# Performance work log

Measured on AMD Instinct MI355X. Metric: run time of the kernel, lower is better.

The kernel has to match this reference:

```python
import jax, jax.numpy as jnp
import numpy as np

B, IN_SEQ, TGT_SEQ = 128, 50, 25
IN_SIZE, OUT_SIZE, RNN = 128, 128, 2048


def setup_inputs() -> dict:
    key = jax.random.key(0)
    ks = jax.random.split(key, 10)
    s_in = 1.0 / np.sqrt(IN_SIZE)
    s_out = 1.0 / np.sqrt(OUT_SIZE)
    s_rnn = 1.0 / np.sqrt(RNN)
    return {
        "encoder_inputs": jax.random.normal(ks[0], (B, IN_SEQ, IN_SIZE), jnp.float32),
        "decoder_inputs": jax.random.normal(ks[1], (B, TGT_SEQ, IN_SIZE), jnp.float32),
        "fc1_w": jax.random.uniform(ks[2], (OUT_SIZE, IN_SIZE), jnp.float32, -s_in, s_in),
        "fc1_b": jax.random.uniform(ks[3], (OUT_SIZE,), jnp.float32, -s_in, s_in),
        "w_ih": jax.random.uniform(ks[4], (3 * RNN, OUT_SIZE), jnp.float32, -s_rnn, s_rnn),
        "w_hh": jax.random.uniform(ks[5], (3 * RNN, RNN), jnp.float32, -s_rnn, s_rnn),
        "b_ih": jax.random.uniform(ks[6], (3 * RNN,), jnp.float32, -s_rnn, s_rnn),
        "b_hh": jax.random.uniform(ks[7], (3 * RNN,), jnp.float32, -s_rnn, s_rnn),
        "fc2_w": jax.random.uniform(ks[8], (OUT_SIZE, RNN), jnp.float32, -s_rnn, s_rnn),
        "fc2_b": jax.random.uniform(ks[9], (OUT_SIZE,), jnp.float32, -s_rnn, s_rnn),
    }


def _gru_cell(x, h, w_ih, w_hh, b_ih, b_hh):
    # PyTorch GRUCell: gates ordered (r, z, n)
    gi = x @ w_ih.T + b_ih            # [B, 3R]
    gh = h @ w_hh.T + b_hh            # [B, 3R]
    i_r, i_z, i_n = jnp.split(gi, 3, axis=-1)
    h_r, h_z, h_n = jnp.split(gh, 3, axis=-1)
    r = jax.nn.sigmoid(i_r + h_r)
    z = jax.nn.sigmoid(i_z + h_z)
    n = jnp.tanh(i_n + r * h_n)
    return (1.0 - z) * n + z * h


def reference(encoder_inputs, decoder_inputs, fc1_w, fc1_b, w_ih, w_hh, b_ih, b_hh, fc2_w, fc2_b):
    # Eval mode: F.dropout(training=False) is identity.
    enc = encoder_inputs @ fc1_w.T + fc1_b              # [B, S_in, OUT]
    enc_t = jnp.transpose(enc, (1, 0, 2))               # time-major [S_in, B, OUT]
    h0 = jnp.zeros((encoder_inputs.shape[0], RNN), enc.dtype)

    def enc_step(state, x):
        return _gru_cell(x, state, w_ih, w_hh, b_ih, b_hh), None

    state, _ = jax.lax.scan(enc_step, h0, enc_t[:-1])   # input_seq - 1 steps

    def dec_step(carry, _):
        state, inp = carry
        inp = jax.lax.stop_gradient(inp)                # inp.detach()
        state = _gru_cell(inp, state, w_ih, w_hh, b_ih, b_hh)
        out = inp + state @ fc2_w.T + fc2_b             # residual decoder
        return (state, out), out

    _, outs = jax.lax.scan(dec_step, (state, enc_t[-1]), None, length=TGT_SEQ)
    return jnp.transpose(outs, (1, 0, 2))               # [B, TGT_SEQ, OUT]
```

## Files before the change

kernel.cpp:

```cpp
#include <hip/hip_runtime.h>
#include <limits.h>

constexpr int kB   = 128;
constexpr int kSin = 50;
constexpr int kT   = 25;
constexpr int kD   = 128;
constexpr int kR   = 2048;
constexpr int kNB  = 256;
constexpr int kNT  = 512;
constexpr int kRing = 8;

typedef __bf16 bf16x8 __attribute__((ext_vector_type(8)));
typedef float  f32x4  __attribute__((ext_vector_type(4)));
typedef unsigned short u16;
typedef unsigned long long u64;

__device__ __forceinline__ float bf2f(u16 u){ union{unsigned i; float f;}x; x.i=((unsigned)u)<<16; return x.f; }
__device__ __forceinline__ u16 f2bf(float f){ union{float f; unsigned i;}x; x.f=f; return (u16)((x.i + 0x7FFFu + ((x.i>>16)&1u))>>16); }
__device__ __forceinline__ float sigm(float x){ return 1.f/(1.f+__expf(-x)); }
__device__ __forceinline__ float tanhf_fast(float x){ return 1.f - 2.f/(__expf(2.f*x)+1.f); }

__device__ __forceinline__ void stg32(unsigned* p, unsigned v){
    __hip_atomic_store(p, v, __ATOMIC_RELAXED, __HIP_MEMORY_SCOPE_AGENT);
}
__device__ __forceinline__ void stg64(u64* p, u64 v){
    __hip_atomic_store(p, v, __ATOMIC_RELAXED, __HIP_MEMORY_SCOPE_AGENT);
}
__device__ __forceinline__ unsigned ald32(const void* p){
    return __hip_atomic_load((const unsigned*)p, __ATOMIC_RELAXED, __HIP_MEMORY_SCOPE_AGENT);
}
__device__ __forceinline__ u64 ald64(const void* p){
    return __hip_atomic_load((const u64*)p, __ATOMIC_RELAXED, __HIP_MEMORY_SCOPE_AGENT);
}
__device__ __forceinline__ bf16x8 ald128bf(const u16* p){
    union{ u64 q[2]; bf16x8 v; } t;
    t.q[0] = ald64(p);
    t.q[1] = ald64(p + 4);
    return t.v;
}
__device__ __forceinline__ float aldf(const float* p){
    union{ unsigned u; float f; } t; t.u = ald32(p); return t.f;
}

__device__ __forceinline__ bf16x8 pack8(float4 a, float4 b){
    union{ bf16x8 v; u16 u[8]; } t;
    t.u[0]=f2bf(a.x); t.u[1]=f2bf(a.y); t.u[2]=f2bf(a.z); t.u[3]=f2bf(a.w);
    t.u[4]=f2bf(b.x); t.u[5]=f2bf(b.y); t.u[6]=f2bf(b.z); t.u[7]=f2bf(b.w);
    return t.v;
}

__device__ __forceinline__ int pollflag(int* flags, int idx, int iter){
    if ((iter & 4095) == 4095) return atomicMax(&flags[idx*16], INT_MIN);
    return (int)ald32(&flags[idx*16]);
}
__device__ __forceinline__ void wait16(int* flags, int k, int base){
    const int lane = threadIdx.x & 63;
    for (int iter = 0;; ++iter){
        bool ok = true;
        if (lane < 16) ok = (pollflag(flags, base + lane, iter) >= k);
        if (__ballot(ok) == ~0ull) return;
        __builtin_amdgcn_s_sleep(4);
    }
}
__device__ __forceinline__ void wait128(int* flags, int k, int base){
    const int lane = threadIdx.x & 63;
    for (int iter = 0;; ++iter){
        bool ok = true;
#pragma unroll
        for (int j = 0; j < 2; ++j)
            ok &= (pollflag(flags, base + lane*2 + j, iter) >= k);
        if (__ballot(ok) == ~0ull) return;
        __builtin_amdgcn_s_sleep(4);
    }
}
__device__ __forceinline__ void arrive(int* flags, int k){
    __syncthreads();
    if (threadIdx.x == 0) stg32((unsigned*)&flags[blockIdx.x*16], (unsigned)k);
}

__device__ __forceinline__ void gbar(int* flags, int k, int base, int perlane)
{
    __syncthreads();
    const int tid = threadIdx.x;
    if (tid == 0) atomicMax(&flags[blockIdx.x*16], k);
    if (tid < 64) {
        int iter = 0;
        for (;;) {
            bool ok = true;
            for (int j = 0; j < perlane; ++j) {
                const int idx = base + tid*perlane + j;
                int v;
                if ((iter & 511) == 511) v = atomicMax(&flags[idx*16], INT_MIN);
                else                     v = (int)ald32(&flags[idx*16]);
                ok &= (v >= k);
            }
            if (__ballot(ok) == ~0ull) break;
            ++iter;
            __builtin_amdgcn_s_sleep(2);
        }
    }
    __syncthreads();
}

__device__ __forceinline__ void cvt_f32_bf16(const float* __restrict__ s, u16* __restrict__ d,
                                             int n4, int gtid, int gstride)
{
    for (int i = gtid; i < n4; i += gstride) {
        float4 v = ((const float4*)s)[i];
        u64 pk = (u64)f2bf(v.x) | ((u64)f2bf(v.y)<<16) | ((u64)f2bf(v.z)<<32) | ((u64)f2bf(v.w)<<48);
        stg64((u64*)d + i, pk);
    }
}

template<int NT, int NACC>
__device__ __forceinline__ void small_gemm(
    const u16* __restrict__ Am, int alda,
    const u16* __restrict__ Bp, int bldb,
    f32x4 (&acc)[NACC], u16* pool)
{
    const int tid=threadIdx.x, lane=tid&63, wv=tid>>6, g=wv>>2, mt=wv&3, ar=lane&15, aq=lane>>4;
    u16* sA = pool;
    u16* sB = pool + 8704;
    { int q=tid,     r=q>>4, c=q&15; *(uint4*)&sA[r*136+c*8] = *(const uint4*)(Am + r*alda + c*8); }
    { int q=tid+512, r=q>>4, c=q&15; *(uint4*)&sA[r*136+c*8] = *(const uint4*)(Am + r*alda + c*8); }
    for (int q=tid; q<NT*256; q+=kNT){
        int r=q>>4, c=q&15;
        *(uint4*)&sB[r*136+c*8] = *(const uint4*)(Bp + (size_t)r*bldb + c*8);
    }
    __syncthreads();
#pragma unroll
    for (int jt=0; jt<NT; ++jt){
        if ((jt&1) != g) continue;
#pragma unroll
        for (int kk=0; kk<4; ++kk){
            bf16x8 a = *(const bf16x8*)&sA[(mt*16+ar)*136 + kk*32 + aq*8];
            bf16x8 b = *(const bf16x8*)&sB[(jt*16+ar)*136 + kk*32 + aq*8];
            acc[jt>>1] = __builtin_amdgcn_mfma_f32_16x16x32_bf16(a,b,acc[jt>>1],0,0,0);
        }
    }
    __syncthreads();
}

__device__ __forceinline__ void gru_phase_flag(
    const u16* __restrict__ hcur, u16* __restrict__ hnxt,
    const u16* __restrict__ xb,
    const bf16x8 (&wB)[3][8], const bf16x8 (&wI)[3],
    const float4 b4, float (&hprev)[4],
    int wgc, int mrow0, u16* smem, u16* sH,
    int* flags, int hk, int xk, int fbase, bool dofence, int setk)
{
    const int tid=threadIdx.x, lane=tid&63, w=tid>>6, ar=lane&15, aq=lane>>4;
    const f32x4 zz = {0.f,0.f,0.f,0.f};
    f32x4 acc[3][4] = {{zz,zz,zz,zz},{zz,zz,zz,zz},{zz,zz,zz,zz}};
    f32x4 xn[4] = {zz,zz,zz,zz};

    if (dofence) __builtin_amdgcn_fence(__ATOMIC_ACQUIRE, "agent");

    if (hk) wait16(flags, hk, fbase + 16*w);

#pragma unroll
    for (int mt=0; mt<4; ++mt){
        const int row = mrow0 + mt*16 + ar;
        bf16x8 af[8];
#pragma unroll
        for (int c=0; c<8; ++c){
            const int s = 16*w + 2*c + (aq>>1);
            af[c] = *(const bf16x8*)(hcur + (((s*128 + row)<<4) + (aq&1)*8));
        }
#pragma unroll
        for (int c=0; c<8; ++c){
            acc[0][mt] = __builtin_amdgcn_mfma_f32_16x16x32_bf16(af[c], wB[0][c], acc[0][mt],0,0,0);
            acc[1][mt] = __builtin_amdgcn_mfma_f32_16x16x32_bf16(af[c], wB[1][c], acc[1][mt],0,0,0);
            acc[2][mt] = __builtin_amdgcn_mfma_f32_16x16x32_bf16(af[c], wB[2][c], acc[2][mt],0,0,0);
        }
    }
    if (w < 4){
        if (xk) wait128(flags, xk, fbase);
#pragma unroll
        for (int mt=0; mt<4; ++mt){
            bf16x8 ax = *(const bf16x8*)(xb + (mrow0+mt*16+ar)*kD + 32*w + aq*8);
            acc[0][mt] = __builtin_amdgcn_mfma_f32_16x16x32_bf16(ax, wI[0], acc[0][mt],0,0,0);
            acc[1][mt] = __builtin_amdgcn_mfma_f32_16x16x32_bf16(ax, wI[1], acc[1][mt],0,0,0);
            xn[mt]     = __builtin_amdgcn_mfma_f32_16x16x32_bf16(ax, wI[2], xn[mt],0,0,0);
        }
    }
    float* red = (float*)smem;
#define RCELL(wp,g4,mt) (red + (((((wp)*4+(g4))*4+(mt))*64 + lane)<<2))
    if (w >= 4){
#pragma unroll
        for (int g=0; g<3; ++g)
#pragma unroll
            for (int mt=0; mt<4; ++mt)
                *(f32x4*)RCELL(w-4, g, mt) = acc[g][mt];
    }
    __syncthreads();
    if (w < 4){
#pragma unroll
        for (int g=0; g<3; ++g)
#pragma unroll
            for (int mt=0; mt<4; ++mt)
                acc[g][mt] += *(f32x4*)RCELL(w, g, mt);
#pragma unroll
        for (int g=0; g<3; ++g)
#pragma unroll
            for (int mt=0; mt<4; ++mt)
                *(f32x4*)RCELL(w, g, mt) = acc[g][mt];
#pragma unroll
        for (int mt=0; mt<4; ++mt)
            *(f32x4*)RCELL(w, 3, mt) = xn[mt];
    }
    __syncthreads();
    if (tid < 256){
        const int mt = tid>>6, ls = tid&63, aqs = ls>>4, ars = ls&15;
        f32x4 R=zz, Z=zz, NH=zz, NX=zz;
#pragma unroll
        for (int wp=0; wp<4; ++wp){
            R  += *(f32x4*)(red + ((((wp*4+0)*4+mt)*64 + ls)<<2));
            Z  += *(f32x4*)(red + ((((wp*4+1)*4+mt)*64 + ls)<<2));
            NH += *(f32x4*)(red + ((((wp*4+2)*4+mt)*64 + ls)<<2));
            NX += *(f32x4*)(red + ((((wp*4+3)*4+mt)*64 + ls)<<2));
        }
#pragma unroll
        for (int rr=0; rr<4; ++rr){
            const int m = mrow0 + mt*16 + aqs*4 + rr;
            float r_ = sigm(R[rr] + b4.x);
            float z_ = sigm(Z[rr] + b4.y);
            float n_ = tanhf_fast(NX[rr] + b4.z + r_*(NH[rr] + b4.w));
            float hn = (1.f-z_)*n_ + z_*hprev[rr];
            hprev[rr] = hn;
            u16 hb = f2bf(hn);
            sH[(mt*16 + aqs*4 + rr)*16 + ars] = hb;
            unsigned other = (unsigned)__shfl_xor((int)(unsigned)hb, 1);
            if (!(ars&1))
                stg32((unsigned*)(hnxt + ((wgc*128+m)<<4) + ars), (unsigned)hb | (other<<16));
        }
    }
#undef RCELL
    __syncthreads();
    if (setk && tid == 0) stg32((unsigned*)&flags[blockIdx.x*16], (unsigned)setk);
}

__device__ __forceinline__ void fc2_partial(
    const u16* __restrict__ sH, const bf16x8 (&wF2)[4],
    int wgc, int mh, float* __restrict__ part)
{
    const int tid=threadIdx.x, lane=tid&63, w=tid>>6, ar=lane&15, aq=lane>>4;
    const int mt = w&3, nh = w>>2;
    bf16x8 a;
    if (aq < 2) a = *(const bf16x8*)&sH[(mt*16+ar)*16 + aq*8];
    else {
#pragma unroll
        for (int i=0;i<8;++i) a[i] = (__bf16)0.f;
    }
    const f32x4 zz = {0.f,0.f,0.f,0.f};
    f32x4 acc[4] = {zz,zz,zz,zz};
#pragma unroll
    for (int j=0;j<4;++j)
        acc[j] = __builtin_amdgcn_mfma_f32_16x16x32_bf16(a, wF2[j], acc[j],0,0,0);
#pragma unroll
    for (int j=0;j<4;++j){
        const int col = (nh*4+j)*16 + ar;
#pragma unroll
        for (int rr=0;rr<4;++rr){
            const int row = mt*16 + aq*4 + rr;
            stg32((unsigned*)(part + ((((size_t)mh*64+row)*128 + wgc)*128 + col)),
                  __float_as_uint(acc[j][rr]));
        }
    }
}

__global__ __launch_bounds__(kNT, 2) void seq2seq_kernel(
    const void* __restrict__ enc_in_raw, const void* __restrict__ fc1_w_raw,
    const void* __restrict__ fc1_b_raw,  const void* __restrict__ w_ih_raw,
    const void* __restrict__ w_hh_raw,   const void* __restrict__ b_ih_raw,
    const void* __restrict__ b_hh_raw,   const void* __restrict__ fc2_w_raw,
    const void* __restrict__ fc2_b_raw,
    void* __restrict__ out_raw,
    u16* __restrict__ enc_act,
    u16* __restrict__ h_b16,
    u16* __restrict__ inp_b16,
    float* __restrict__ inp_f32,
    float* __restrict__ encF,
    float* __restrict__ bias,
    float* __restrict__ part,
    int* flags,
    u16* __restrict__ cv_encx, u16* __restrict__ cv_fc2, u16* __restrict__ cv_fc1)
{
    __shared__ __align__(16) u16 smem[33792];
    __shared__ int sflag;
    u16* sH = smem + 32768;
    const int wg = blockIdx.x, tid = threadIdx.x;
    const int wgc = wg & 127, mrow0 = (wg >> 7) * 64;
    const int lane = tid & 63, wv = tid >> 6, ar = lane & 15, aq = lane >> 4;
    const int gtid = wg * kNT + tid, gstride = kNB * kNT;
    const int dom = (wg >> 7) * 128;
    const size_t HS = (size_t)kB*kR;

    {
        const u16* p = (const u16*)enc_in_raw;
        int found = 0;
        for (int i = tid; i < 16384; i += kNT) found |= ((p[i] & 0x7F80) == 0x7F80) ? 1 : 0;
        if (tid == 0) sflag = 0;
        __syncthreads();
        if (found) sflag = 1;
        __syncthreads();
    }
    const bool F32 = (sflag != 0);

    bf16x8 wB[3][8];
    bf16x8 wI[3];
    {
        const int w4 = wv & 3;
        if (F32){
            const float* Wh = (const float*)w_hh_raw;
            const float* Wi = (const float*)w_ih_raw;
#pragma unroll
            for (int g=0; g<3; ++g)
#pragma unroll
                for (int c=0; c<8; ++c){
                    size_t o = (size_t)(g*kR + wgc*16 + ar)*kR + 256*wv + 32*c + aq*8;
                    wB[g][c] = pack8(*(const float4*)(Wh+o), *(const float4*)(Wh+o+4));
                }
#pragma unroll
            for (int g=0; g<3; ++g){
                size_t o = (size_t)(g*kR + wgc*16 + ar)*kD + 32*w4 + aq*8;
                wI[g] = pack8(*(const float4*)(Wi+o), *(const float4*)(Wi+o+4));
            }
        } else {
            const u16* Wh = (const u16*)w_hh_raw;
            const u16* Wi = (const u16*)w_ih_raw;
#pragma unroll
            for (int g=0; g<3; ++g)
#pragma unroll
                for (int c=0; c<8; ++c)
                    wB[g][c] = *(const bf16x8*)(Wh + (size_t)(g*kR + wgc*16 + ar)*kR + 256*wv + 32*c + aq*8);
#pragma unroll
            for (int g=0; g<3; ++g)
                wI[g] = *(const bf16x8*)(Wi + (size_t)(g*kR + wgc*16 + ar)*kD + 32*w4 + aq*8);
        }
    }

    if (F32) {
        cvt_f32_bf16((const float*)fc2_w_raw, cv_fc2,  (kD*kR)/4,       gtid, gstride);
        cvt_f32_bf16((const float*)fc1_w_raw, cv_fc1,  (kD*kD)/4,       gtid, gstride);
        cvt_f32_bf16((const float*)enc_in_raw,cv_encx, (kB*kSin*kD)/4,  gtid, gstride);
        for (int i = gtid; i < 3*kR; i += gstride) {
            stg32((unsigned*)&bias[i],        __float_as_uint(((const float*)b_ih_raw)[i]));
            stg32((unsigned*)&bias[3*kR + i], __float_as_uint(((const float*)b_hh_raw)[i]));
        }
        for (int i = gtid; i < kD; i += gstride) {
            stg32((unsigned*)&bias[6*kR + i],      __float_as_uint(((const float*)fc1_b_raw)[i]));
            stg32((unsigned*)&bias[6*kR + kD + i], __float_as_uint(((const float*)fc2_b_raw)[i]));
        }
    } else {
        for (int i = gtid; i < 3*kR; i += gstride) {
            stg32((unsigned*)&bias[i],        __float_as_uint(bf2f(((const u16*)b_ih_raw)[i])));
            stg32((unsigned*)&bias[3*kR + i], __float_as_uint(bf2f(((const u16*)b_hh_raw)[i])));
        }
        for (int i = gtid; i < kD; i += gstride) {
            stg32((unsigned*)&bias[6*kR + i],      __float_as_uint(bf2f(((const u16*)fc1_b_raw)[i])));
            stg32((unsigned*)&bias[6*kR + kD + i], __float_as_uint(bf2f(((const u16*)fc2_b_raw)[i])));
        }
    }
    for (int i = gtid; i < (int)((kB*kR)/2); i += gstride) stg32((unsigned*)h_b16 + i, 0u);
    gbar(flags, 1, 0, 4);

    const u16* ENCX = F32 ? cv_encx : (const u16*)enc_in_raw;
    const u16* WF2  = F32 ? cv_fc2  : (const u16*)fc2_w_raw;
    const u16* WF1  = F32 ? cv_fc1  : (const u16*)fc1_w_raw;

    float4 b4;
    {
        const int hc = wgc*16 + ar;
        b4.x = aldf(&bias[hc])      + aldf(&bias[3*kR+hc]);
        b4.y = aldf(&bias[kR+hc])   + aldf(&bias[4*kR+hc]);
        b4.z = aldf(&bias[2*kR+hc]);
        b4.w = aldf(&bias[5*kR+hc]);
    }
    bf16x8 wF2[4];
    {
        const int nh = wv>>2;
#pragma unroll
        for (int j=0;j<4;++j){
            if (aq < 2)
                wF2[j] = ald128bf(WF2 + (size_t)((nh*4+j)*16+ar)*kR + wgc*16 + aq*8);
            else {
#pragma unroll
                for (int i=0;i<8;++i) wF2[j][i] = (__bf16)0.f;
            }
        }
    }
    const float fc2b = aldf(&bias[6*kR + kD + (wg&1)*64 + (tid&63)]);
    float hprev[4] = {0.f, 0.f, 0.f, 0.f};

    if (wgc < kSin) {
        const int g = wv>>2, mt = wv&3;
        const f32x4 zz = {0.f,0.f,0.f,0.f};
        f32x4 ae[4] = {zz,zz,zz,zz};
        small_gemm<8,4>(ENCX + ((size_t)mrow0*kSin + wgc)*kD, kSin*kD, WF1, kD, ae, smem);
#pragma unroll
        for (int jt=0; jt<8; ++jt){
            if ((jt&1) != g) continue;
            int col = jt*16 + ar;
            float fb = aldf(&bias[6*kR + col]);
#pragma unroll
            for (int rr=0; rr<4; ++rr){
                int m = mrow0 + mt*16 + aq*4 + rr;
                float v = ae[jt>>1][rr] + fb;
                u16 hb = f2bf(v);
                unsigned other = (unsigned)__shfl_xor((int)(unsigned)hb, 1);
                if (!(ar&1))
                    stg32((unsigned*)(enc_act + ((size_t)wgc*kB + m)*kD + col),
                          (unsigned)hb | (other<<16));
                if (wgc == kSin-1)
                    stg32((unsigned*)(encF + (size_t)m*kD + col), __float_as_uint(v));
            }
        }
    }
    gbar(flags, 2, dom, 2);

    for (int t = 0; t < kSin-1; ++t) {
        gru_phase_flag(h_b16 + (size_t)(t & 7)*HS, h_b16 + (size_t)((t+1) & 7)*HS,
                       enc_act + (size_t)t*kB*kD, wB, wI, b4, hprev, wgc, mrow0, smem, sH,
                       flags, (t==0 ? 0 : t+2), 0, dom,
                       (t > 0) && ((t & 7) == 0), t+3);
    }

    const u16*   ib  = enc_act + (size_t)(kSin-1)*kB*kD;
    const float* ifp = encF;
    const int mh = wg >> 7;
    for (int d = 0; d < kT; ++d) {
        const int g = 49 + d;
        gru_phase_flag(h_b16 + (size_t)(g & 7)*HS, h_b16 + (size_t)((g+1) & 7)*HS,
                       ib, wB, wI, b4, hprev, wgc, mrow0, smem, sH,
                       flags, (d==0 ? 51 : 49+3*d), (d==0 ? 0 : 51+3*d), dom,
                       (g & 7) == 0, 52+3*d);
        fc2_partial(sH, wF2, wgc, mh, part);
        arrive(flags, 53+3*d);

        u16*   nib = inp_b16 + (size_t)(d & 7)*kB*kD;
        float* nif = inp_f32 + (size_t)(d & 7)*kB*kD;
        wait128(flags, 53+3*d, dom);
        {
            const int row = wg >> 1, ch = wg & 1;
            const int mh2 = row >> 6, rl = row & 63;
            const float* pr = part + (size_t)((mh2*64 + rl)*128)*128;
            const int cl = tid & 63, sg = tid >> 6;
            float s = 0.f;
#pragma unroll
            for (int j=0;j<16;++j) s += aldf(&pr[(size_t)(sg*16+j)*128 + ch*64 + cl]);
            float* red2 = (float*)smem;
            red2[sg*64 + cl] = s;
            __syncthreads();
            if (tid < 64){
                float t2 = 0.f;
#pragma unroll
                for (int g2=0; g2<8; ++g2) t2 += red2[g2*64 + tid];
                const int colg = ch*64 + tid;
                const float o = t2 + fc2b + aldf(&ifp[(size_t)row*kD + colg]);
                const size_t ob = ((size_t)row*kT + d)*kD + colg;
                if (F32) ((float*)out_raw)[ob] = o;
                else     ((u16*)out_raw)[ob]   = f2bf(o);
                stg32((unsigned*)(nif + (size_t)row*kD + colg), __float_as_uint(o));
                u16 hb = f2bf(o);
                unsigned other = (unsigned)__shfl_xor((int)(unsigned)hb, 1);
                if (!(tid&1))
                    stg32((unsigned*)(nib + (size_t)row*kD + colg), (unsigned)hb | (other<<16));
            }
        }
        arrive(flags, 54+3*d);
        ib = nib; ifp = nif;
    }
}

extern "C" void kernel_launch(void* const* d_in, const int* in_sizes, int n_in,
                              void* d_out, int out_size, void* d_ws, size_t ws_size,
                              hipStream_t stream)
{
    size_t off = 0;
    char* ws = (char*)d_ws;
    auto alloc = [&](size_t bytes) -> char* {
        char* p = ws + off;
        off = (off + bytes + 255) & ~(size_t)255;
        return p;
    };
    u16*   enc_act = (u16*)alloc((size_t)kSin*kB*kD*2);
    u16*   h_b16   = (u16*)alloc((size_t)kRing*kB*kR*2);
    u16*   inp_b16 = (u16*)alloc((size_t)kRing*kB*kD*2);
    float* inp_f32 = (float*)alloc((size_t)kRing*kB*kD*4);
    float* encF    = (float*)alloc((size_t)kB*kD*4);
    float* bias    = (float*)alloc((size_t)(6*kR + 2*kD)*4);
    float* part    = (float*)alloc((size_t)2*64*128*128*4);
    int*   flags   = (int*)alloc((size_t)kNB*16*4);
    u16*   cv_encx = (u16*)alloc((size_t)kB*kSin*kD*2);
    u16*   cv_fc2  = (u16*)alloc((size_t)kD*kR*2);
    u16*   cv_fc1  = (u16*)alloc((size_t)kD*kD*2);
    (void)ws_size; (void)in_sizes; (void)n_in; (void)out_size;

    seq2seq_kernel<<<dim3(kNB), dim3(kNT), 0, stream>>>(
        d_in[0], d_in[2], d_in[3], d_in[4], d_in[5], d_in[6], d_in[7], d_in[8], d_in[9],
        d_out,
        enc_act, h_b16, inp_b16, inp_f32, encF, bias, part, flags,
        cv_encx, cv_fc2, cv_fc1);
}
```

Baseline: 1.518 ms.

## Fold fc2 into decoder GRU input weights and defer fc2 output projection

The decoder input at step d equals the encoder input plus a running sum of fc2(h) terms. This lets the GRU input projection be rewritten as W_ih·fc2_w applied to h, plus a precomputed constant and an accumulated vector. The combined weights (wM) are precomputed per block and applied in the same MFMA pass as W_hh. This removes the per-step fc2 partial-sum exchange and its two extra grid-wide flag syncs, leaving one sync per decoder step. Hidden states are saved to a history buffer and fc2 plus the residual sum are computed after the loop, at the cost of double the per-step MFMA work, a slow scalar precompute of wM, and bf16 rounding of the folded weights.

```diff
diff --git a/kernel.cpp b/kernel.cpp
--- a/kernel.cpp
+++ b/kernel.cpp
@@ -29,15 +29,6 @@
 __device__ __forceinline__ unsigned ald32(const void* p){
     return __hip_atomic_load((const unsigned*)p, __ATOMIC_RELAXED, __HIP_MEMORY_SCOPE_AGENT);
 }
-__device__ __forceinline__ u64 ald64(const void* p){
-    return __hip_atomic_load((const u64*)p, __ATOMIC_RELAXED, __HIP_MEMORY_SCOPE_AGENT);
-}
-__device__ __forceinline__ bf16x8 ald128bf(const u16* p){
-    union{ u64 q[2]; bf16x8 v; } t;
-    t.q[0] = ald64(p);
-    t.q[1] = ald64(p + 4);
-    return t.v;
-}
 __device__ __forceinline__ float aldf(const float* p){
     union{ unsigned u; float f; } t; t.u = ald32(p); return t.f;
 }
@@ -62,22 +53,6 @@
         __builtin_amdgcn_s_sleep(4);
     }
 }
-__device__ __forceinline__ void wait128(int* flags, int k, int base){
-    const int lane = threadIdx.x & 63;
-    for (int iter = 0;; ++iter){
-        bool ok = true;
-#pragma unroll
-        for (int j = 0; j < 2; ++j)
-            ok &= (pollflag(flags, base + lane*2 + j, iter) >= k);
-        if (__ballot(ok) == ~0ull) return;
-        __builtin_amdgcn_s_sleep(4);
-    }
-}
-__device__ __forceinline__ void arrive(int* flags, int k){
-    __syncthreads();
-    if (threadIdx.x == 0) stg32((unsigned*)&flags[blockIdx.x*16], (unsigned)k);
-}
-
 __device__ __forceinline__ void gbar(int* flags, int k, int base, int perlane)
 {
     __syncthreads();
@@ -141,13 +116,13 @@
     __syncthreads();
 }
 
-__device__ __forceinline__ void gru_phase_flag(
+__device__ __forceinline__ void gru_phase_enc(
     const u16* __restrict__ hcur, u16* __restrict__ hnxt,
     const u16* __restrict__ xb,
     const bf16x8 (&wB)[3][8], const bf16x8 (&wI)[3],
     const float4 b4, float (&hprev)[4],
-    int wgc, int mrow0, u16* smem, u16* sH,
-    int* flags, int hk, int xk, int fbase, bool dofence, int setk)
+    int wgc, int mrow0, u16* smem,
+    int* flags, int hk, int fbase, bool dofence, int setk)
 {
     const int tid=threadIdx.x, lane=tid&63, w=tid>>6, ar=lane&15, aq=lane>>4;
     const f32x4 zz = {0.f,0.f,0.f,0.f};
@@ -155,7 +130,6 @@
     f32x4 xn[4] = {zz,zz,zz,zz};
 
     if (dofence) __builtin_amdgcn_fence(__ATOMIC_ACQUIRE, "agent");
-
     if (hk) wait16(flags, hk, fbase + 16*w);
 
 #pragma unroll
@@ -175,7 +149,6 @@
         }
     }
     if (w < 4){
-        if (xk) wait128(flags, xk, fbase);
 #pragma unroll
         for (int mt=0; mt<4; ++mt){
             bf16x8 ax = *(const bf16x8*)(xb + (mrow0+mt*16+ar)*kD + 32*w + aq*8);
@@ -229,7 +202,6 @@
             float hn = (1.f-z_)*n_ + z_*hprev[rr];
             hprev[rr] = hn;
             u16 hb = f2bf(hn);
-            sH[(mt*16 + aqs*4 + rr)*16 + ars] = hb;
             unsigned other = (unsigned)__shfl_xor((int)(unsigned)hb, 1);
             if (!(ars&1))
                 stg32((unsigned*)(hnxt + ((wgc*128+m)<<4) + ars), (unsigned)hb | (other<<16));
@@ -240,33 +212,100 @@
     if (setk && tid == 0) stg32((unsigned*)&flags[blockIdx.x*16], (unsigned)setk);
 }
 
-__device__ __forceinline__ void fc2_partial(
-    const u16* __restrict__ sH, const bf16x8 (&wF2)[4],
-    int wgc, int mh, float* __restrict__ part)
+__device__ __forceinline__ void gru_phase_dec(
+    const u16* __restrict__ hcur, u16* __restrict__ hnxt, u16* __restrict__ hist_d,
+    const bf16x8 (&wB)[3][8], const bf16x8 (&wM)[3][8],
+    const float4 b4, const float (&c3)[3], float (&v3)[3][4], float (&hprev)[4],
+    int wgc, int mrow0, u16* smem,
+    int* flags, int hk, int setk, int fbase, bool dofence, bool updv)
 {
     const int tid=threadIdx.x, lane=tid&63, w=tid>>6, ar=lane&15, aq=lane>>4;
-    const int mt = w&3, nh = w>>2;
-    bf16x8 a;
-    if (aq < 2) a = *(const bf16x8*)&sH[(mt*16+ar)*16 + aq*8];
-    else {
-#pragma unroll
-        for (int i=0;i<8;++i) a[i] = (__bf16)0.f;
-    }
     const f32x4 zz = {0.f,0.f,0.f,0.f};
-    f32x4 acc[4] = {zz,zz,zz,zz};
-#pragma unroll
-    for (int j=0;j<4;++j)
-        acc[j] = __builtin_amdgcn_mfma_f32_16x16x32_bf16(a, wF2[j], acc[j],0,0,0);
-#pragma unroll
-    for (int j=0;j<4;++j){
-        const int col = (nh*4+j)*16 + ar;
-#pragma unroll
-        for (int rr=0;rr<4;++rr){
-            const int row = mt*16 + aq*4 + rr;
-            stg32((unsigned*)(part + ((((size_t)mh*64+row)*128 + wgc)*128 + col)),
-                  __float_as_uint(acc[j][rr]));
-        }
-    }
+    f32x4 aH[3][4] = {{zz,zz,zz,zz},{zz,zz,zz,zz},{zz,zz,zz,zz}};
+    f32x4 aM[3][4] = {{zz,zz,zz,zz},{zz,zz,zz,zz},{zz,zz,zz,zz}};
+
+    if (dofence) __builtin_amdgcn_fence(__ATOMIC_ACQUIRE, "agent");
+    if (hk) wait16(flags, hk, fbase + 16*w);
+
+#pragma unroll
+    for (int mt=0; mt<4; ++mt){
+        const int row = mrow0 + mt*16 + ar;
+        bf16x8 af[8];
+#pragma unroll
+        for (int c=0; c<8; ++c){
+            const int s = 16*w + 2*c + (aq>>1);
+            af[c] = *(const bf16x8*)(hcur + (((s*128 + row)<<4) + (aq&1)*8));
+        }
+#pragma unroll
+        for (int c=0; c<8; ++c){
+            aH[0][mt] = __builtin_amdgcn_mfma_f32_16x16x32_bf16(af[c], wB[0][c], aH[0][mt],0,0,0);
+            aH[1][mt] = __builtin_amdgcn_mfma_f32_16x16x32_bf16(af[c], wB[1][c], aH[1][mt],0,0,0);
+            aH[2][mt] = __builtin_amdgcn_mfma_f32_16x16x32_bf16(af[c], wB[2][c], aH[2][mt],0,0,0);
+            aM[0][mt] = __builtin_amdgcn_mfma_f32_16x16x32_bf16(af[c], wM[0][c], aM[0][mt],0,0,0);
+            aM[1][mt] = __builtin_amdgcn_mfma_f32_16x16x32_bf16(af[c], wM[1][c], aM[1][mt],0,0,0);
+            aM[2][mt] = __builtin_amdgcn_mfma_f32_16x16x32_bf16(af[c], wM[2][c], aM[2][mt],0,0,0);
+        }
+    }
+    float* red = (float*)smem;
+#define RC6(wp,q,mt) (red + (((((wp)*6+(q))*4+(mt))*64 + lane)<<2))
+    if (w >= 4){
+#pragma unroll
+        for (int g=0; g<3; ++g)
+#pragma unroll
+            for (int mt=0; mt<4; ++mt){
+                *(f32x4*)RC6(w-4, g,   mt) = aH[g][mt];
+                *(f32x4*)RC6(w-4, g+3, mt) = aM[g][mt];
+            }
+    }
+    __syncthreads();
+    if (w < 4){
+#pragma unroll
+        for (int g=0; g<3; ++g)
+#pragma unroll
+            for (int mt=0; mt<4; ++mt){
+                aH[g][mt] += *(f32x4*)RC6(w, g,   mt);
+                aM[g][mt] += *(f32x4*)RC6(w, g+3, mt);
+                *(f32x4*)RC6(w, g,   mt) = aH[g][mt];
+                *(f32x4*)RC6(w, g+3, mt) = aM[g][mt];
+            }
+    }
+    __syncthreads();
+    if (tid < 256){
+        const int mt = tid>>6, ls = tid&63, aqs = ls>>4, ars = ls&15;
+        f32x4 HR=zz, HZ=zz, HN=zz, MR=zz, MZ=zz, MN=zz;
+#pragma unroll
+        for (int wp=0; wp<4; ++wp){
+            HR += *(f32x4*)(red + ((((wp*6+0)*4+mt)*64 + ls)<<2));
+            HZ += *(f32x4*)(red + ((((wp*6+1)*4+mt)*64 + ls)<<2));
+            HN += *(f32x4*)(red + ((((wp*6+2)*4+mt)*64 + ls)<<2));
+            MR += *(f32x4*)(red + ((((wp*6+3)*4+mt)*64 + ls)<<2));
+            MZ += *(f32x4*)(red + ((((wp*6+4)*4+mt)*64 + ls)<<2));
+            MN += *(f32x4*)(red + ((((wp*6+5)*4+mt)*64 + ls)<<2));
+        }
+#pragma unroll
+        for (int rr=0; rr<4; ++rr){
+            if (updv){
+                v3[0][rr] += c3[0] + MR[rr];
+                v3[1][rr] += c3[1] + MZ[rr];
+                v3[2][rr] += c3[2] + MN[rr];
+            }
+            const int m = mrow0 + mt*16 + aqs*4 + rr;
+            float r_ = sigm(HR[rr] + v3[0][rr] + b4.x);
+            float z_ = sigm(HZ[rr] + v3[1][rr] + b4.y);
+            float n_ = tanhf_fast(v3[2][rr] + b4.z + r_*(HN[rr] + b4.w));
+            float hn = (1.f-z_)*n_ + z_*hprev[rr];
+            hprev[rr] = hn;
+            u16 hb = f2bf(hn);
+            unsigned other = (unsigned)__shfl_xor((int)(unsigned)hb, 1);
+            if (!(ars&1)){
+                stg32((unsigned*)(hnxt + ((wgc*128+m)<<4) + ars), (unsigned)hb | (other<<16));
+                stg32((unsigned*)(hist_d + (size_t)m*kR + wgc*16 + ars), (unsigned)hb | (other<<16));
+            }
+        }
+    }
+#undef RC6
+    __syncthreads();
+    if (setk && tid == 0) stg32((unsigned*)&flags[blockIdx.x*16], (unsigned)setk);
 }
 
 __global__ __launch_bounds__(kNT, 2) void seq2seq_kernel(
@@ -278,17 +317,16 @@
     void* __restrict__ out_raw,
     u16* __restrict__ enc_act,
     u16* __restrict__ h_b16,
-    u16* __restrict__ inp_b16,
-    float* __restrict__ inp_f32,
+    u16* __restrict__ hist,
+    float* __restrict__ Fbuf,
+    u16* __restrict__ fc2T,
     float* __restrict__ encF,
     float* __restrict__ bias,
-    float* __restrict__ part,
     int* flags,
-    u16* __restrict__ cv_encx, u16* __restrict__ cv_fc2, u16* __restrict__ cv_fc1)
+    u16* __restrict__ cv_encx, u16* __restrict__ cv_fc1)
 {
-    __shared__ __align__(16) u16 smem[33792];
+    __shared__ __align__(16) u16 smem[49152];
     __shared__ int sflag;
-    u16* sH = smem + 32768;
     const int wg = blockIdx.x, tid = threadIdx.x;
     const int wgc = wg & 127, mrow0 = (wg >> 7) * 64;
     const int lane = tid & 63, wv = tid >> 6, ar = lane & 15, aq = lane >> 4;
@@ -341,7 +379,6 @@
     }
 
     if (F32) {
-        cvt_f32_bf16((const float*)fc2_w_raw, cv_fc2,  (kD*kR)/4,       gtid, gstride);
         cvt_f32_bf16((const float*)fc1_w_raw, cv_fc1,  (kD*kD)/4,       gtid, gstride);
         cvt_f32_bf16((const float*)enc_in_raw,cv_encx, (kB*kSin*kD)/4,  gtid, gstride);
         for (int i = gtid; i < 3*kR; i += gstride) {
@@ -352,6 +389,13 @@
             stg32((unsigned*)&bias[6*kR + i],      __float_as_uint(((const float*)fc1_b_raw)[i]));
             stg32((unsigned*)&bias[6*kR + kD + i], __float_as_uint(((const float*)fc2_b_raw)[i]));
         }
+        const float* F2 = (const float*)fc2_w_raw;
+        for (int i = gtid; i < (kR*kD)/2; i += gstride){
+            int k = i >> 6, jp = i & 63;
+            unsigned lo = f2bf(F2[(size_t)(2*jp  )*kR + k]);
+            unsigned hi = f2bf(F2[(size_t)(2*jp+1)*kR + k]);
+            stg32((unsigned*)fc2T + (size_t)k*64 + jp, lo | (hi<<16));
+        }
     } else {
         for (int i = gtid; i < 3*kR; i += gstride) {
             stg32((unsigned*)&bias[i],        __float_as_uint(bf2f(((const u16*)b_ih_raw)[i])));
@@ -361,13 +405,55 @@
             stg32((unsigned*)&bias[6*kR + i],      __float_as_uint(bf2f(((const u16*)fc1_b_raw)[i])));
             stg32((unsigned*)&bias[6*kR + kD + i], __float_as_uint(bf2f(((const u16*)fc2_b_raw)[i])));
         }
+        const u16* F2 = (const u16*)fc2_w_raw;
+        for (int i = gtid; i < (kR*kD)/2; i += gstride){
+            int k = i >> 6, jp = i & 63;
+            unsigned lo = F2[(size_t)(2*jp  )*kR + k];
+            unsigned hi = F2[(size_t)(2*jp+1)*kR + k];
+            stg32((unsigned*)fc2T + (size_t)k*64 + jp, lo | (hi<<16));
+        }
     }
     for (int i = gtid; i < (int)((kB*kR)/2); i += gstride) stg32((unsigned*)h_b16 + i, 0u);
     gbar(flags, 1, 0, 4);
 
     const u16* ENCX = F32 ? cv_encx : (const u16*)enc_in_raw;
-    const u16* WF2  = F32 ? cv_fc2  : (const u16*)fc2_w_raw;
     const u16* WF1  = F32 ? cv_fc1  : (const u16*)fc1_w_raw;
+
+    bf16x8 wM[3][8];
+    {
+#pragma unroll
+        for (int g=0; g<3; ++g){
+            const size_t wroff = (size_t)(g*kR + wgc*16 + ar)*kD;
+#pragma unroll
+            for (int c=0; c<8; ++c){
+                const int kb = 256*wv + 32*c + aq*8;
+                float a8[8] = {0.f,0.f,0.f,0.f,0.f,0.f,0.f,0.f};
+                for (int j=0; j<kD; j+=8){
+                    float wj[8];
+                    if (F32){
+                        const float* wr = (const float*)w_ih_raw + wroff + j;
+#pragma unroll
+                        for (int q2=0;q2<8;++q2) wj[q2] = wr[q2];
+                    } else {
+                        const u16* wr = (const u16*)w_ih_raw + wroff + j;
+#pragma unroll
+                        for (int q2=0;q2<8;++q2) wj[q2] = bf2f(wr[q2]);
+                    }
+#pragma unroll
+                    for (int i=0;i<8;++i){
+                        union{ bf16x8 v; u16 u[8]; } f8;
+                        f8.v = *(const bf16x8*)(fc2T + (size_t)(kb+i)*kD + j);
+#pragma unroll
+                        for (int q2=0;q2<8;++q2) a8[i] += wj[q2] * bf2f(f8.u[q2]);
+                    }
+                }
+                union{ bf16x8 v; u16 u[8]; } pk;
+#pragma unroll
+                for (int i=0;i<8;++i) pk.u[i] = f2bf(a8[i]);
+                wM[g][c] = pk.v;
+            }
+        }
+    }
 
     float4 b4;
     {
@@ -377,20 +463,6 @@
         b4.z = aldf(&bias[2*kR+hc]);
         b4.w = aldf(&bias[5*kR+hc]);
     }
-    bf16x8 wF2[4];
-    {
-        const int nh = wv>>2;
-#pragma unroll
-        for (int j=0;j<4;++j){
-            if (aq < 2)
-                wF2[j] = ald128bf(WF2 + (size_t)((nh*4+j)*16+ar)*kR + wgc*16 + aq*8);
-            else {
-#pragma unroll
-                for (int i=0;i<8;++i) wF2[j][i] = (__bf16)0.f;
-            }
-        }
-    }
-    const float fc2b = aldf(&bias[6*kR + kD + (wg&1)*64 + (tid&63)]);
     float hprev[4] = {0.f, 0.f, 0.f, 0.f};
 
     if (wgc < kSin) {
@@ -420,56 +492,93 @@
     gbar(flags, 2, dom, 2);
 
     for (int t = 0; t < kSin-1; ++t) {
-        gru_phase_flag(h_b16 + (size_t)(t & 7)*HS, h_b16 + (size_t)((t+1) & 7)*HS,
-                       enc_act + (size_t)t*kB*kD, wB, wI, b4, hprev, wgc, mrow0, smem, sH,
-                       flags, (t==0 ? 0 : t+2), 0, dom,
-                       (t > 0) && ((t & 7) == 0), t+3);
-    }
-
-    const u16*   ib  = enc_act + (size_t)(kSin-1)*kB*kD;
-    const float* ifp = encF;
-    const int mh = wg >> 7;
+        gru_phase_enc(h_b16 + (size_t)(t & 7)*HS, h_b16 + (size_t)((t+1) & 7)*HS,
+                      enc_act + (size_t)t*kB*kD, wB, wI, b4, hprev, wgc, mrow0, smem,
+                      flags, (t==0 ? 0 : t+2), dom, (t > 0) && ((t & 7) == 0), t+3);
+    }
+
+    float v3[3][4] = {{0,0,0,0},{0,0,0,0},{0,0,0,0}};
+    float c3[3] = {0.f,0.f,0.f};
+    if (tid < 256){
+        const int mtp = tid>>6, aqp = (tid&63)>>4, arp = tid&15;
+        const int hc = wgc*16 + arp;
+#pragma unroll
+        for (int g=0; g<3; ++g){
+            float cacc = 0.f, va0=0.f, va1=0.f, va2=0.f, va3=0.f;
+            const int m0 = mrow0 + mtp*16 + aqp*4;
+            if (F32){
+                const float* wr = (const float*)w_ih_raw + (size_t)(g*kR + hc)*kD;
+                for (int j=0;j<kD;++j){
+                    float wj = wr[j];
+                    cacc += wj * bias[6*kR + kD + j];
+                    va0 += wj * encF[(size_t)(m0+0)*kD + j];
+                    va1 += wj * encF[(size_t)(m0+1)*kD + j];
+                    va2 += wj * encF[(size_t)(m0+2)*kD + j];
+                    va3 += wj * encF[(size_t)(m0+3)*kD + j];
+                }
+            } else {
+                const u16* wr = (const u16*)w_ih_raw + (size_t)(g*kR + hc)*kD;
+                for (int j=0;j<kD;++j){
+                    float wj = bf2f(wr[j]);
+                    cacc += wj * bias[6*kR + kD + j];
+                    va0 += wj * encF[(size_t)(m0+0)*kD + j];
+                    va1 += wj * encF[(size_t)(m0+1)*kD + j];
+                    va2 += wj * encF[(size_t)(m0+2)*kD + j];
+                    va3 += wj * encF[(size_t)(m0+3)*kD + j];
+                }
+            }
+            c3[g] = cacc;
+            v3[g][0]=va0; v3[g][1]=va1; v3[g][2]=va2; v3[g][3]=va3;
+        }
+    }
+
     for (int d = 0; d < kT; ++d) {
         const int g = 49 + d;
-        gru_phase_flag(h_b16 + (size_t)(g & 7)*HS, h_b16 + (size_t)((g+1) & 7)*HS,
-                       ib, wB, wI, b4, hprev, wgc, mrow0, smem, sH,
-                       flags, (d==0 ? 51 : 49+3*d), (d==0 ? 0 : 51+3*d), dom,
-                       (g & 7) == 0, 52+3*d);
-        fc2_partial(sH, wF2, wgc, mh, part);
-        arrive(flags, 53+3*d);
-
-        u16*   nib = inp_b16 + (size_t)(d & 7)*kB*kD;
-        float* nif = inp_f32 + (size_t)(d & 7)*kB*kD;
-        wait128(flags, 53+3*d, dom);
-        {
-            const int row = wg >> 1, ch = wg & 1;
-            const int mh2 = row >> 6, rl = row & 63;
-            const float* pr = part + (size_t)((mh2*64 + rl)*128)*128;
-            const int cl = tid & 63, sg = tid >> 6;
-            float s = 0.f;
-#pragma unroll
-            for (int j=0;j<16;++j) s += aldf(&pr[(size_t)(sg*16+j)*128 + ch*64 + cl]);
-            float* red2 = (float*)smem;
-            red2[sg*64 + cl] = s;
+        gru_phase_dec(h_b16 + (size_t)(g & 7)*HS, h_b16 + (size_t)((g+1) & 7)*HS,
+                      hist + (size_t)d*kB*kR,
+                      wB, wM, b4, c3, v3, hprev, wgc, mrow0, smem,
+                      flags, 51+d, 52+d, dom, (g & 7) == 0, d > 0);
+    }
+    gbar(flags, 77, 0, 4);
+
+    {
+        float* sF = (float*)smem;
+        const int j = tid & 127, kq = tid >> 7;
+        for (int u = wg; u < kT*kB; u += kNB){
+            const int e = u >> 7, m = u & 127;
+            const u16* hb = hist + (size_t)(e*kB + m)*kR + kq*512;
+            float p = 0.f;
+            for (int kk=0; kk<512; kk+=8){
+                union{ bf16x8 v; u16 u[8]; } hv;
+                hv.v = *(const bf16x8*)(hb + kk);
+#pragma unroll
+                for (int i=0;i<8;++i){
+                    u16 wv2 = fc2T[(size_t)(kq*512+kk+i)*kD + j];
+                    p += bf2f(hv.u[i]) * bf2f(wv2);
+                }
+            }
             __syncthreads();
-            if (tid < 64){
-                float t2 = 0.f;
-#pragma unroll
-                for (int g2=0; g2<8; ++g2) t2 += red2[g2*64 + tid];
-                const int colg = ch*64 + tid;
-                const float o = t2 + fc2b + aldf(&ifp[(size_t)row*kD + colg]);
-                const size_t ob = ((size_t)row*kT + d)*kD + colg;
-                if (F32) ((float*)out_raw)[ob] = o;
-                else     ((u16*)out_raw)[ob]   = f2bf(o);
-                stg32((unsigned*)(nif + (size_t)row*kD + colg), __float_as_uint(o));
-                u16 hb = f2bf(o);
-                unsigned other = (unsigned)__shfl_xor((int)(unsigned)hb, 1);
-                if (!(tid&1))
-                    stg32((unsigned*)(nib + (size_t)row*kD + colg), (unsigned)hb | (other<<16));
-            }
-        }
-        arrive(flags, 54+3*d);
-        ib = nib; ifp = nif;
+            sF[tid] = p;
+            __syncthreads();
+            if (tid < 128){
+                float s = sF[tid] + sF[128+tid] + sF[256+tid] + sF[384+tid];
+                stg32((unsigned*)&Fbuf[(size_t)(e*kB+m)*kD + tid], __float_as_uint(s));
+            }
+        }
+    }
+    gbar(flags, 78, 0, 4);
+
+    if (wg < 32){
+        const int id = wg*kNT + tid;
+        const int m = id >> 7, j = id & 127;
+        float acc = encF[(size_t)m*kD + j];
+        const float fb = bias[6*kR + kD + j];
+        for (int e=0; e<kT; ++e){
+            acc += Fbuf[(size_t)(e*kB + m)*kD + j] + fb;
+            const size_t ob = ((size_t)m*kT + e)*kD + j;
+            if (F32) ((float*)out_raw)[ob] = acc;
+            else     ((u16*)out_raw)[ob]   = f2bf(acc);
+        }
     }
 }
 
@@ -486,20 +595,19 @@
     };
     u16*   enc_act = (u16*)alloc((size_t)kSin*kB*kD*2);
     u16*   h_b16   = (u16*)alloc((size_t)kRing*kB*kR*2);
-    u16*   inp_b16 = (u16*)alloc((size_t)kRing*kB*kD*2);
-    float* inp_f32 = (float*)alloc((size_t)kRing*kB*kD*4);
+    u16*   hist    = (u16*)alloc((size_t)kT*kB*kR*2);
+    float* Fbuf    = (float*)alloc((size_t)kT*kB*kD*4);
+    u16*   fc2T    = (u16*)alloc((size_t)kR*kD*2);
     float* encF    = (float*)alloc((size_t)kB*kD*4);
     float* bias    = (float*)alloc((size_t)(6*kR + 2*kD)*4);
-    float* part    = (float*)alloc((size_t)2*64*128*128*4);
     int*   flags   = (int*)alloc((size_t)kNB*16*4);
     u16*   cv_encx = (u16*)alloc((size_t)kB*kSin*kD*2);
-    u16*   cv_fc2  = (u16*)alloc((size_t)kD*kR*2);
     u16*   cv_fc1  = (u16*)alloc((size_t)kD*kD*2);
     (void)ws_size; (void)in_sizes; (void)n_in; (void)out_size;
 
     seq2seq_kernel<<<dim3(kNB), dim3(kNT), 0, stream>>>(
         d_in[0], d_in[2], d_in[3], d_in[4], d_in[5], d_in[6], d_in[7], d_in[8], d_in[9],
         d_out,
-        enc_act, h_b16, inp_b16, inp_f32, encF, bias, part, flags,
-        cv_encx, cv_fc2, cv_fc1);
-}
+        enc_act, h_b16, hist, Fbuf, fc2T, encF, bias, flags,
+        cv_encx, cv_fc1);
+}
```

Result: slower. 3.290 ms (+116.8%).
